# Kernel tuning notes

Measured on AMD Instinct MI355X. Metric: run time of the kernel, lower is better.

Reference implementation:

```python
import jax, jax.numpy as jnp
import numpy as np

B, M, D = 512, 100000, 256
EPS = 1e-8  # torch.cosine_similarity eps
TEMP = 10.0  # softmax temperature from source


def setup_inputs() -> dict:
    key = jax.random.key(0)
    kx, kk, kv = jax.random.split(key, 3)
    x = jax.random.normal(kx, (B, D), dtype=jnp.float32)
    memory_keys = jax.random.normal(kk, (M, D), dtype=jnp.float32) * 0.1
    memory_values = jax.random.normal(kv, (M, D), dtype=jnp.float32) * 0.1
    return {"x": x, "memory_keys": memory_keys, "memory_values": memory_values}


def reference(x, memory_keys, memory_values):
    # cosine similarity between x [B,D] and memory_keys [M,D] -> [B,M]
    dots = jnp.einsum("bd,md->bm", x, memory_keys)
    xn = jnp.linalg.norm(x, axis=-1)          # [B]
    kn = jnp.linalg.norm(memory_keys, axis=-1)  # [M]
    denom = jnp.maximum(xn[:, None] * kn[None, :], EPS)
    sims = dots / denom                         # [B,M]
    attn = jax.nn.softmax(sims * TEMP, axis=-1)  # [B,M]
    retrieved = jnp.einsum("bm,md->bd", attn, memory_values)  # [B,D]
    return retrieved, attn
```

## Files before the change

### kernel.cpp

```cpp
#include <hip/hip_runtime.h>
#include <hip/hip_bf16.h>


#define MCOLS 100000
#define MP    100032
#define DDIM  256
#define CHUNK 1792
#define NTFULL 28
#define NCHUNK 56
#define NST2  112
#define NSLOT 56
#define ATTN_OFF 131072
#define WS_RXN  0
#define WS_RKN  512
#define WS_RCPL 100512
#define WS_XB_BYTE   409600ull
#define WS_VT_BYTE   1048576ull
#define WS_PART_BYTE 52264960ull
#define WS_KB_BYTE   84246528ull
#define WS_KB_END    (WS_KB_BYTE + 2ull*(size_t)MCOLS*DDIM)

#define GLL(g, l) __builtin_amdgcn_global_load_lds( \
    (const __attribute__((address_space(1))) void*)(g), \
    (__attribute__((address_space(3))) void*)(l), 16, 0, 0)

typedef short short8 __attribute__((ext_vector_type(8)));
typedef float f32x4  __attribute__((ext_vector_type(4)));

static __device__ __forceinline__ unsigned short f2bfu(float f) {
  union { __hip_bfloat16 h; unsigned short u; } cv;
  cv.h = __float2bfloat16(f);
  return cv.u;
}
static __device__ __forceinline__ unsigned int pk2(float a, float b) {
  return (unsigned int)f2bfu(a) | ((unsigned int)f2bfu(b) << 16);
}
static __device__ __forceinline__ short8 pack8(float4 a, float4 b) {
  short8 r;
  r[0] = (short)f2bfu(a.x); r[1] = (short)f2bfu(a.y);
  r[2] = (short)f2bfu(a.z); r[3] = (short)f2bfu(a.w);
  r[4] = (short)f2bfu(b.x); r[5] = (short)f2bfu(b.y);
  r[6] = (short)f2bfu(b.z); r[7] = (short)f2bfu(b.w);
  return r;
}

__global__ void k0_xn(const float* __restrict__ x, float* __restrict__ ws) {
  const int b = blockIdx.x, t = threadIdx.x;
  const float v = x[b*DDIM + t];
  float s = v*v;
  #pragma unroll
  for (int mk = 1; mk <= 32; mk <<= 1) s += __shfl_xor(s, mk);
  __shared__ float ps[4];
  if ((t & 63) == 0) ps[t >> 6] = s;
  __syncthreads();
  const float tot = ps[0] + ps[1] + ps[2] + ps[3];
  const float r10 = 10.0f / fmaxf(sqrtf(tot), 1e-12f);
  if (t == 0) ws[WS_RXN + b] = r10;
  unsigned short* xbp = (unsigned short*)((char*)ws + WS_XB_BYTE);
  xbp[b*DDIM + t] = f2bfu(v * r10);
}

template<bool WRITEKB>
__global__ __launch_bounds__(256) void k0c_kn(const float* __restrict__ K,
                                              float* __restrict__ ws) {
  const int t = threadIdx.x;
  const int mg = blockIdx.x*64 + (t >> 2);
  const int qq = t & 3;
  if (mg >= MCOLS) return;
  const float* kp = K + (size_t)mg*DDIM + 64*qq;
  float4 buf[16];
  float ss = 0.f;
  #pragma unroll
  for (int j = 0; j < 16; ++j) {
    buf[j] = *(const float4*)(kp + 4*j);
    ss += buf[j].x*buf[j].x + buf[j].y*buf[j].y + buf[j].z*buf[j].z + buf[j].w*buf[j].w;
  }
  ss += __shfl_xor(ss, 1); ss += __shfl_xor(ss, 2);
  const float rk = 1.0f / fmaxf(sqrtf(ss), 1e-12f);
  if (qq == 0) ws[WS_RKN + mg] = rk;
  if (WRITEKB) {
    unsigned int* kb = (unsigned int*)((char*)ws + WS_KB_BYTE);
    #pragma unroll
    for (int j = 0; j < 8; ++j) {
      const float4 a = buf[2*j], b2 = buf[2*j+1];
      uint4 u;
      u.x = pk2(a.x*rk, a.y*rk);  u.y = pk2(a.z*rk, a.w*rk);
      u.z = pk2(b2.x*rk, b2.y*rk); u.w = pk2(b2.z*rk, b2.w*rk);
      const int slot = (8*qq + j) ^ (mg & 7);
      *(uint4*)(kb + (size_t)mg*128 + slot*4) = u;
    }
  }
}

__global__ __launch_bounds__(256) void k0b_tr(const float* __restrict__ V,
                                              float* __restrict__ ws) {
  const int t = threadIdx.x;
  const int m0 = blockIdx.x * 64;
  __shared__ float vt_f[64][261];
  #pragma unroll
  for (int i = 0; i < 4; ++i) {
    const int ml = (t >> 4) + 16*i;
    const int mg = m0 + ml;
    #pragma unroll
    for (int j = 0; j < 4; ++j) {
      const int d = 4*(t & 15) + 64*j;
      float4 v = make_float4(0.f, 0.f, 0.f, 0.f);
      if (mg < MCOLS) v = *(const float4*)(V + (size_t)mg*DDIM + d);
      vt_f[ml][d] = v.x; vt_f[ml][d+1] = v.y; vt_f[ml][d+2] = v.z; vt_f[ml][d+3] = v.w;
    }
  }
  __syncthreads();
  unsigned short* vt = (unsigned short*)((char*)ws + WS_VT_BYTE);
  const int tl = t & 15;
  const int s = tl >> 1, hf = tl & 1;
  const int mq = 8*s + 4*hf;
  #pragma unroll
  for (int it = 0; it < 16; ++it) {
    const int d = (t >> 4) + 16*it;
    uint2 u;
    u.x = pk2(vt_f[mq+0][d], vt_f[mq+1][d]);
    u.y = pk2(vt_f[mq+2][d], vt_f[mq+3][d]);
    const int sp = s ^ (d & 7);
    *(uint2*)(vt + (size_t)d*MP + m0 + sp*8 + 4*hf) = u;
  }
}

static __device__ __forceinline__ void stage_k(const char* __restrict__ kb,
                                               int m0, int w, int l,
                                               unsigned short (*klds)[256]) {
  #pragma unroll
  for (int i = 0; i < 4; ++i) {
    int r = m0 + w*8 + i*2 + (l >> 5);
    r = min(r, MCOLS - 1);
    const char* g = kb + (size_t)r*512 + (l & 31)*16;
    char* dst = (char*)&klds[w*8 + i*2][0];
    GLL(g, dst);
  }
}
static __device__ __forceinline__ void stage_vt(const char* __restrict__ vtb,
                                                int m1, int w, int l,
                                                unsigned short (*vtl)[64]) {
  #pragma unroll
  for (int i = 0; i < 4; ++i) {
    const int d = w*32 + i*8 + (l >> 3);
    const int ms = min(m1 + (l & 7)*8, MP - 8);
    const char* g = vtb + ((size_t)d*MP + ms)*2;
    char* dst = (char*)&vtl[w*32 + i*8][0];
    GLL(g, dst);
  }
}

__global__ __launch_bounds__(512, 4) void k1b_sum(const float* __restrict__ ws,
                                                  float* __restrict__ out) {
  const int bid = blockIdx.x;
  const int xg = bid & 7, i = bid >> 3;
  const int c = xg + 8*(i % 7), rb = i / 7;
  const int t = threadIdx.x, w = t >> 6, l = t & 63, q = l >> 4, ln = l & 15;
  const int ar = w & 3, h = w >> 2, l7 = ln & 7;
  __shared__ __align__(16) unsigned short klds2[2][64][256];
  const char* kb = (const char*)ws + WS_KB_BYTE;
  const unsigned short* xb = (const unsigned short*)((const char*)ws + WS_XB_BYTE);
  const int R0 = rb*64;

  short8 xf[8];
  {
    const int row = R0 + 16*ar + ln;
    #pragma unroll
    for (int kk = 0; kk < 8; ++kk)
      xf[kk] = *(const short8*)(xb + row*DDIM + 32*kk + 8*q);
  }
  float lpr[4] = {0.f,0.f,0.f,0.f};
  const int mbase = c*CHUNK;
  const int nt = min(NTFULL, (MCOLS - mbase + 63) >> 6);

  stage_k(kb, mbase, w, l, klds2[0]);
  __syncthreads();
  for (int mt = 0; mt < nt; ++mt) {
    const int cur = mt & 1;
    const int m0 = mbase + mt*64;
    if (mt + 1 < nt) stage_k(kb, m0 + 64, w, l, klds2[cur ^ 1]);
    const char* kbase = (const char*)&klds2[cur][0][0];
    const int row0 = 32*h + ln;
    f32x4 acc[2];
    { f32x4 z = {0.f,0.f,0.f,0.f}; acc[0] = z; acc[1] = z; }
    #pragma unroll
    for (int kk = 0; kk < 8; ++kk) {
      const int sl = ((q + 4*kk) ^ l7) << 4;
      const short8 b0 = *(const short8*)(kbase + row0*512 + sl);
      const short8 b1 = *(const short8*)(kbase + (row0 + 16)*512 + sl);
      acc[0] = __builtin_amdgcn_mfma_f32_16x16x32_bf16(xf[kk], b0, acc[0], 0,0,0);
      acc[1] = __builtin_amdgcn_mfma_f32_16x16x32_bf16(xf[kk], b1, acc[1], 0,0,0);
    }
    const int mr0 = m0 + row0, mr1 = mr0 + 16;
    const bool ok0 = mr0 < MCOLS, ok1 = mr1 < MCOLS;
    #pragma unroll
    for (int r = 0; r < 4; ++r)
      lpr[r] += (ok0 ? __expf(acc[0][r]) : 0.f) + (ok1 ? __expf(acc[1][r]) : 0.f);
    __syncthreads();
  }
  #pragma unroll
  for (int r = 0; r < 4; ++r) {
    float s = lpr[r];
    s += __shfl_xor(s, 1); s += __shfl_xor(s, 2);
    s += __shfl_xor(s, 4); s += __shfl_xor(s, 8);
    if (ln == 0)
      out[(size_t)(c*2 + h)*512 + R0 + 16*ar + 4*q + r] = s;
  }
}

__global__ void k2_final(const float* __restrict__ out, float* __restrict__ ws) {
  const int b = blockIdx.x, t = threadIdx.x;
  float v = (t < NST2) ? out[(size_t)t*512 + b] : 0.f;
  #pragma unroll
  for (int mk = 1; mk <= 32; mk <<= 1) v += __shfl_xor(v, mk);
  __shared__ float s2[2];
  if ((t & 63) == 0) s2[t >> 6] = v;
  __syncthreads();
  if (t == 0) ws[WS_RCPL + b] = 1.0f / (s2[0] + s2[1]);
}

__global__ __launch_bounds__(512, 4) void k3a_main(float* __restrict__ ws,
                                                   float* __restrict__ out) {
  const int bid = blockIdx.x;
  const int xg = bid & 7, i = bid >> 3;
  const int c = xg + 8*(i % 7), rb = i / 7;
  const int t = threadIdx.x, w = t >> 6, l = t & 63, q = l >> 4, ln = l & 15;
  const int ar = w & 3, h = w >> 2, l7 = ln & 15 & 7;
  __shared__ __align__(16) unsigned short klds[64][256];
  __shared__ __align__(16) unsigned short vtl[256][64];
  __shared__ __align__(16) unsigned short plds[64][64];
  const char* kb  = (const char*)ws + WS_KB_BYTE;
  const char* vtb = (const char*)ws + WS_VT_BYTE;
  const unsigned short* xb = (const unsigned short*)((const char*)ws + WS_XB_BYTE);
  const int R0 = rb*64;

  short8 xf[8];
  {
    const int row = R0 + 16*ar + ln;
    #pragma unroll
    for (int kk = 0; kk < 8; ++kk)
      xf[kk] = *(const short8*)(xb + row*DDIM + 32*kk + 8*q);
  }
  float rlq[4];
  #pragma unroll
  for (int r = 0; r < 4; ++r)
    rlq[r] = ws[WS_RCPL + R0 + 16*ar + 4*q + r];
  f32x4 apv[8];
  #pragma unroll
  for (int dx = 0; dx < 8; ++dx) { f32x4 z = {0.f,0.f,0.f,0.f}; apv[dx] = z; }
  const int d2 = 128*h;
  float* attn = out + ATTN_OFF;
  const int mbase = c*CHUNK;
  const int nt = min(NTFULL, (MCOLS - mbase + 63) >> 6);
  unsigned short* pf = &plds[0][0];

  stage_k(kb, mbase, w, l, klds);
  __syncthreads();

  for (int mt = 0; mt < nt; ++mt) {
    const int m0 = mbase + mt*64;
    stage_vt(vtb, m0, w, l, vtl);
    const int row0 = 32*h + ln;
    f32x4 acc[2];
    { f32x4 z = {0.f,0.f,0.f,0.f}; acc[0] = z; acc[1] = z; }
    #pragma unroll
    for (int kk = 0; kk < 8; ++kk) {
      const int sl = ((q + 4*kk) ^ l7) << 4;
      const short8 b0 = *(const short8*)((const char*)&klds[0][0] + row0*512 + sl);
      const short8 b1 = *(const short8*)((const char*)&klds[0][0] + (row0 + 16)*512 + sl);
      acc[0] = __builtin_amdgcn_mfma_f32_16x16x32_bf16(xf[kk], b0, acc[0], 0,0,0);
      acc[1] = __builtin_amdgcn_mfma_f32_16x16x32_bf16(xf[kk], b1, acc[1], 0,0,0);
    }
    const int mr0 = m0 + row0, mr1 = mr0 + 16;
    const bool ok0 = mr0 < MCOLS, ok1 = mr1 < MCOLS;
    #pragma unroll
    for (int r = 0; r < 4; ++r) {
      const int rowl = 16*ar + 4*q + r;
      const float p0v = ok0 ? __expf(acc[0][r]) : 0.f;
      const float p1v = ok1 ? __expf(acc[1][r]) : 0.f;
      float* arow = attn + (size_t)(R0 + rowl)*MCOLS;
      if (ok0) arow[mr0] = p0v*rlq[r];
      if (ok1) arow[mr1] = p1v*rlq[r];
      const int r7 = rowl & 7;
      pf[rowl*64 + ((((ln>>3) + 4*h    ) ^ r7) << 3) + (ln & 7)] = f2bfu(p0v);
      pf[rowl*64 + ((((ln>>3) + 4*h + 2) ^ r7) << 3) + (ln & 7)] = f2bfu(p1v);
    }
    __syncthreads();
    if (mt + 1 < nt) stage_k(kb, m0 + 64, w, l, klds);
    const int prow = 16*ar + ln;
    const short8 af0 = *(const short8*)(pf + prow*64 + ((q       ^ l7) << 3));
    const short8 af1 = *(const short8*)(pf + prow*64 + (((4 + q) ^ l7) << 3));
    #pragma unroll
    for (int dx = 0; dx < 8; ++dx) {
      const int R = d2 + 16*dx + ln;
      const char* vr = (const char*)&vtl[0][0] + R*128;
      const short8 bv0 = *(const short8*)(vr + ((q       ^ l7) << 4));
      const short8 bv1 = *(const short8*)(vr + (((4 + q) ^ l7) << 4));
      apv[dx] = __builtin_amdgcn_mfma_f32_16x16x32_bf16(af0, bv0, apv[dx], 0,0,0);
      apv[dx] = __builtin_amdgcn_mfma_f32_16x16x32_bf16(af1, bv1, apv[dx], 0,0,0);
    }
    __syncthreads();
  }

  float* part = (float*)((char*)ws + WS_PART_BYTE);
  #pragma unroll
  for (int dx = 0; dx < 8; ++dx)
    #pragma unroll
    for (int r = 0; r < 4; ++r)
      part[((size_t)c*512 + R0 + 16*ar + 4*q + r)*256 + d2 + 16*dx + ln]
        = apv[dx][r]*rlq[r];
}

static __device__ __forceinline__ void load_xf(const float* __restrict__ x,
                                               int brow0, int q, int ln,
                                               short8 xf[2][8]) {
  #pragma unroll
  for (int as = 0; as < 2; ++as) {
    const int row = brow0 + 16*as + ln;
    #pragma unroll
    for (int kk = 0; kk < 8; ++kk) {
      const float* p = x + row*DDIM + 32*kk + 8*q;
      xf[as][kk] = pack8(*(const float4*)p, *(const float4*)(p + 4));
    }
  }
}

__global__ __launch_bounds__(512, 2) void k3b_main(const float* __restrict__ x,
                                                   const float* __restrict__ K,
                                                   float* __restrict__ ws,
                                                   float* __restrict__ out) {
  const int bid = blockIdx.x;
  const int c = bid >> 2, rb = bid & 3;
  const int t = threadIdx.x, w = t >> 6, l = t & 63, q = l >> 4, ln = l & 15;
  const int h = w & 1, rg = w >> 1;
  __shared__ __align__(16) unsigned short plds[2][128][72];
  const int R0 = rb*128;
  short8 xf[2][8];
  const int brow0 = R0 + 32*rg;
  load_xf(x, brow0, q, ln, xf);
  float rxn[2][4];
  #pragma unroll
  for (int as = 0; as < 2; ++as)
    #pragma unroll
    for (int r = 0; r < 4; ++r)
      rxn[as][r] = ws[WS_RXN + brow0 + 16*as + 4*q + r];
  float lpr[2][4] = {{0.f,0.f,0.f,0.f},{0.f,0.f,0.f,0.f}};
  f32x4 apv[2][8];
  #pragma unroll
  for (int bs = 0; bs < 2; ++bs)
    #pragma unroll
    for (int dx = 0; dx < 8; ++dx) { f32x4 z = {0.f,0.f,0.f,0.f}; apv[bs][dx] = z; }
  const int b2 = 32*(w & 3), d2 = 128*(w >> 2);
  const unsigned short* vt = (const unsigned short*)((const char*)ws + WS_VT_BYTE);
  const float* rknw = ws + WS_RKN;
  float* attn = out + ATTN_OFF;
  const int mbase = c*CHUNK;
  const int nt = min(NTFULL, (MCOLS - mbase + 63) >> 6);
  const int l7 = ln & 7;

  for (int mt = 0; mt < nt; ++mt) {
    const int m0 = mbase + mt*64;
    const int mr0 = m0 + 32*h + ln, mr1 = mr0 + 16;
    const int kr0 = min(mr0, MCOLS-1), kr1 = min(mr1, MCOLS-1);
    f32x4 acc[2][2];
    #pragma unroll
    for (int as = 0; as < 2; ++as)
      #pragma unroll
      for (int mm = 0; mm < 2; ++mm) { f32x4 z = {0.f,0.f,0.f,0.f}; acc[as][mm] = z; }
    const float* p0 = K + (size_t)kr0*DDIM + 8*q;
    const float* p1 = K + (size_t)kr1*DDIM + 8*q;
    #pragma unroll
    for (int kk = 0; kk < 8; ++kk) {
      const short8 b0 = pack8(*(const float4*)(p0 + 32*kk), *(const float4*)(p0 + 32*kk + 4));
      const short8 b1 = pack8(*(const float4*)(p1 + 32*kk), *(const float4*)(p1 + 32*kk + 4));
      acc[0][0] = __builtin_amdgcn_mfma_f32_16x16x32_bf16(xf[0][kk], b0, acc[0][0], 0,0,0);
      acc[0][1] = __builtin_amdgcn_mfma_f32_16x16x32_bf16(xf[0][kk], b1, acc[0][1], 0,0,0);
      acc[1][0] = __builtin_amdgcn_mfma_f32_16x16x32_bf16(xf[1][kk], b0, acc[1][0], 0,0,0);
      acc[1][1] = __builtin_amdgcn_mfma_f32_16x16x32_bf16(xf[1][kk], b1, acc[1][1], 0,0,0);
    }
    const float rk0 = rknw[kr0], rk1 = rknw[kr1];
    const bool ok0 = mr0 < MCOLS, ok1 = mr1 < MCOLS;
    #pragma unroll
    for (int as = 0; as < 2; ++as)
      #pragma unroll
      for (int r = 0; r < 4; ++r) {
        const int rowl = 32*rg + 16*as + 4*q + r;
        const float p0v = ok0 ? __expf(acc[as][0][r]*rxn[as][r]*rk0) : 0.f;
        const float p1v = ok1 ? __expf(acc[as][1][r]*rxn[as][r]*rk1) : 0.f;
        float* arow = attn + (size_t)(R0 + rowl)*MCOLS;
        if (ok0) arow[mr0] = p0v;
        if (ok1) arow[mr1] = p1v;
        lpr[as][r] += p0v + p1v;
        plds[mt & 1][rowl][32*h + ln]      = f2bfu(p0v);
        plds[mt & 1][rowl][32*h + 16 + ln] = f2bfu(p1v);
      }
    __syncthreads();
    const unsigned short (*pb)[72] = plds[mt & 1];
    const short8 af00 = *(const short8*)&pb[b2 + ln][8*q];
    const short8 af01 = *(const short8*)&pb[b2 + ln][32 + 8*q];
    const short8 af10 = *(const short8*)&pb[b2 + 16 + ln][8*q];
    const short8 af11 = *(const short8*)&pb[b2 + 16 + ln][32 + 8*q];
    #pragma unroll
    for (int dx = 0; dx < 8; ++dx) {
      const int R = d2 + 16*dx + ln;
      const size_t rbase = (size_t)R*MP + m0;
      const short8 bv0 = *(const short8*)(vt + rbase + ((q     ^ (R & 7)) << 3));
      const short8 bv1 = *(const short8*)(vt + rbase + (((4+q) ^ (R & 7)) << 3));
      apv[0][dx] = __builtin_amdgcn_mfma_f32_16x16x32_bf16(af00, bv0, apv[0][dx], 0,0,0);
      apv[0][dx] = __builtin_amdgcn_mfma_f32_16x16x32_bf16(af01, bv1, apv[0][dx], 0,0,0);
      apv[1][dx] = __builtin_amdgcn_mfma_f32_16x16x32_bf16(af10, bv0, apv[1][dx], 0,0,0);
      apv[1][dx] = __builtin_amdgcn_mfma_f32_16x16x32_bf16(af11, bv1, apv[1][dx], 0,0,0);
    }
  }

  #pragma unroll
  for (int as = 0; as < 2; ++as)
    #pragma unroll
    for (int r = 0; r < 4; ++r) {
      float s = lpr[as][r];
      s += __shfl_xor(s, 1); s += __shfl_xor(s, 2);
      s += __shfl_xor(s, 4); s += __shfl_xor(s, 8);
      if (ln == 0)
        out[(size_t)(c*2 + h)*512 + brow0 + 16*as + 4*q + r] = s;
    }
  float* part = (float*)((char*)ws + WS_PART_BYTE);
  #pragma unroll
  for (int bs = 0; bs < 2; ++bs)
    #pragma unroll
    for (int dx = 0; dx < 8; ++dx)
      #pragma unroll
      for (int r = 0; r < 4; ++r)
        part[((size_t)c*512 + R0 + b2 + 16*bs + 4*q + r)*256 + d2 + 16*dx + ln]
          = apv[bs][dx][r];
}

template<bool NORM>
__global__ void k4_red(const float* __restrict__ ws, float* __restrict__ out) {
  const int b = blockIdx.x, t = threadIdx.x;
  const float* part = (const float*)((const char*)ws + WS_PART_BYTE);
  float acc = 0.f;
  for (int cc = 0; cc < NSLOT; ++cc)
    acc += part[((size_t)cc*512 + b)*256 + t];
  if (!NORM) acc *= ws[WS_RCPL + b];
  out[b*DDIM + t] = acc;
}

__global__ void k5_scale(const float* __restrict__ ws, float* __restrict__ out) {
  const int row = blockIdx.y;
  const int i4 = blockIdx.x*256 + threadIdx.x;
  if (i4 >= MCOLS/4) return;
  const float s = ws[WS_RCPL + row];
  float4* p = (float4*)(out + ATTN_OFF + (size_t)row*MCOLS) + i4;
  float4 v = *p;
  v.x *= s; v.y *= s; v.z *= s; v.w *= s;
  *p = v;
}

extern "C" void kernel_launch(void* const* d_in, const int* in_sizes, int n_in,
                              void* d_out, int out_size, void* d_ws, size_t ws_size,
                              hipStream_t stream) {
  const float* x = (const float*)d_in[0];
  const float* K = (const float*)d_in[1];
  const float* V = (const float*)d_in[2];
  float* out = (float*)d_out;
  float* ws  = (float*)d_ws;
  const bool useKB = ws_size >= WS_KB_END;

  k0_xn<<<512, 256, 0, stream>>>(x, ws);
  if (useKB) k0c_kn<true ><<<1563, 256, 0, stream>>>(K, ws);
  else       k0c_kn<false><<<1563, 256, 0, stream>>>(K, ws);
  k0b_tr<<<MP/64, 256, 0, stream>>>(V, ws);
  if (useKB) {
    k1b_sum<<<448, 512, 0, stream>>>(ws, out);
    k2_final<<<512, 128, 0, stream>>>(out, ws);
    k3a_main<<<448, 512, 0, stream>>>(ws, out);
    k4_red<true><<<512, 256, 0, stream>>>(ws, out);
  } else {
    k3b_main<<<224, 512, 0, stream>>>(x, K, ws, out);
    k2_final<<<512, 128, 0, stream>>>(out, ws);
    k5_scale<<<dim3((MCOLS/4 + 255)/256, 512), 256, 0, stream>>>(ws, out);
    k4_red<false><<<512, 256, 0, stream>>>(ws, out);
  }
}
```

Baseline: 250.2 us.

## Fuse softmax denominator pass into main kernel and normalize attention afterwards

Drops the separate exp-sum pass (k1b_sum) that recomputed x·K and exp before the main pass. The main kernel now accumulates the row sums itself and writes unnormalized exp values to attn and to the partial P·V buffers. k5_scale then rescales the full attention matrix, and k4_red applies the reciprocal to the retrieved output. The attn global stores are also moved after the barrier so they overlap with staging the next K tile. The trade-off is that one recompute of the similarity GEMM is exchanged for an extra read and write of the 512×100000 fp32 attention matrix.

```diff
diff --git a/kernel.cpp b/kernel.cpp
--- a/kernel.cpp
+++ b/kernel.cpp
@@ -150,82 +150,24 @@
   }
 }
 
-__global__ __launch_bounds__(512, 4) void k1b_sum(const float* __restrict__ ws,
-                                                  float* __restrict__ out) {
+__global__ void k2_final(const float* __restrict__ out, float* __restrict__ ws) {
+  const int b = blockIdx.x, t = threadIdx.x;
+  float v = (t < NST2) ? out[(size_t)t*512 + b] : 0.f;
+  #pragma unroll
+  for (int mk = 1; mk <= 32; mk <<= 1) v += __shfl_xor(v, mk);
+  __shared__ float s2[2];
+  if ((t & 63) == 0) s2[t >> 6] = v;
+  __syncthreads();
+  if (t == 0) ws[WS_RCPL + b] = 1.0f / (s2[0] + s2[1]);
+}
+
+__global__ __launch_bounds__(512, 4) void k3s_main(float* __restrict__ ws,
+                                                   float* __restrict__ out) {
   const int bid = blockIdx.x;
   const int xg = bid & 7, i = bid >> 3;
   const int c = xg + 8*(i % 7), rb = i / 7;
   const int t = threadIdx.x, w = t >> 6, l = t & 63, q = l >> 4, ln = l & 15;
   const int ar = w & 3, h = w >> 2, l7 = ln & 7;
-  __shared__ __align__(16) unsigned short klds2[2][64][256];
-  const char* kb = (const char*)ws + WS_KB_BYTE;
-  const unsigned short* xb = (const unsigned short*)((const char*)ws + WS_XB_BYTE);
-  const int R0 = rb*64;
-
-  short8 xf[8];
-  {
-    const int row = R0 + 16*ar + ln;
-    #pragma unroll
-    for (int kk = 0; kk < 8; ++kk)
-      xf[kk] = *(const short8*)(xb + row*DDIM + 32*kk + 8*q);
-  }
-  float lpr[4] = {0.f,0.f,0.f,0.f};
-  const int mbase = c*CHUNK;
-  const int nt = min(NTFULL, (MCOLS - mbase + 63) >> 6);
-
-  stage_k(kb, mbase, w, l, klds2[0]);
-  __syncthreads();
-  for (int mt = 0; mt < nt; ++mt) {
-    const int cur = mt & 1;
-    const int m0 = mbase + mt*64;
-    if (mt + 1 < nt) stage_k(kb, m0 + 64, w, l, klds2[cur ^ 1]);
-    const char* kbase = (const char*)&klds2[cur][0][0];
-    const int row0 = 32*h + ln;
-    f32x4 acc[2];
-    { f32x4 z = {0.f,0.f,0.f,0.f}; acc[0] = z; acc[1] = z; }
-    #pragma unroll
-    for (int kk = 0; kk < 8; ++kk) {
-      const int sl = ((q + 4*kk) ^ l7) << 4;
-      const short8 b0 = *(const short8*)(kbase + row0*512 + sl);
-      const short8 b1 = *(const short8*)(kbase + (row0 + 16)*512 + sl);
-      acc[0] = __builtin_amdgcn_mfma_f32_16x16x32_bf16(xf[kk], b0, acc[0], 0,0,0);
-      acc[1] = __builtin_amdgcn_mfma_f32_16x16x32_bf16(xf[kk], b1, acc[1], 0,0,0);
-    }
-    const int mr0 = m0 + row0, mr1 = mr0 + 16;
-    const bool ok0 = mr0 < MCOLS, ok1 = mr1 < MCOLS;
-    #pragma unroll
-    for (int r = 0; r < 4; ++r)
-      lpr[r] += (ok0 ? __expf(acc[0][r]) : 0.f) + (ok1 ? __expf(acc[1][r]) : 0.f);
-    __syncthreads();
-  }
-  #pragma unroll
-  for (int r = 0; r < 4; ++r) {
-    float s = lpr[r];
-    s += __shfl_xor(s, 1); s += __shfl_xor(s, 2);
-    s += __shfl_xor(s, 4); s += __shfl_xor(s, 8);
-    if (ln == 0)
-      out[(size_t)(c*2 + h)*512 + R0 + 16*ar + 4*q + r] = s;
-  }
-}
-
-__global__ void k2_final(const float* __restrict__ out, float* __restrict__ ws) {
-  const int b = blockIdx.x, t = threadIdx.x;
-  float v = (t < NST2) ? out[(size_t)t*512 + b] : 0.f;
-  #pragma unroll
-  for (int mk = 1; mk <= 32; mk <<= 1) v += __shfl_xor(v, mk);
-  __shared__ float s2[2];
-  if ((t & 63) == 0) s2[t >> 6] = v;
-  __syncthreads();
-  if (t == 0) ws[WS_RCPL + b] = 1.0f / (s2[0] + s2[1]);
-}
-
-__global__ __launch_bounds__(512, 4) void k3a_main(float* __restrict__ ws,
-                                                   float* __restrict__ out) {
-  const int bid = blockIdx.x;
-  const int xg = bid & 7, i = bid >> 3;
-  const int c = xg + 8*(i % 7), rb = i / 7;
-  const int t = threadIdx.x, w = t >> 6, l = t & 63, q = l >> 4, ln = l & 15;
-  const int ar = w & 3, h = w >> 2, l7 = ln & 15 & 7;
   __shared__ __align__(16) unsigned short klds[64][256];
   __shared__ __align__(16) unsigned short vtl[256][64];
   __shared__ __align__(16) unsigned short plds[64][64];
@@ -241,10 +183,7 @@
     for (int kk = 0; kk < 8; ++kk)
       xf[kk] = *(const short8*)(xb + row*DDIM + 32*kk + 8*q);
   }
-  float rlq[4];
-  #pragma unroll
-  for (int r = 0; r < 4; ++r)
-    rlq[r] = ws[WS_RCPL + R0 + 16*ar + 4*q + r];
+  float lpr[4] = {0.f,0.f,0.f,0.f};
   f32x4 apv[8];
   #pragma unroll
   for (int dx = 0; dx < 8; ++dx) { f32x4 z = {0.f,0.f,0.f,0.f}; apv[dx] = z; }
@@ -273,20 +212,27 @@
     }
     const int mr0 = m0 + row0, mr1 = mr0 + 16;
     const bool ok0 = mr0 < MCOLS, ok1 = mr1 < MCOLS;
+    float pv0[4], pv1[4];
     #pragma unroll
     for (int r = 0; r < 4; ++r) {
       const int rowl = 16*ar + 4*q + r;
       const float p0v = ok0 ? __expf(acc[0][r]) : 0.f;
       const float p1v = ok1 ? __expf(acc[1][r]) : 0.f;
-      float* arow = attn + (size_t)(R0 + rowl)*MCOLS;
-      if (ok0) arow[mr0] = p0v*rlq[r];
-      if (ok1) arow[mr1] = p1v*rlq[r];
+      pv0[r] = p0v; pv1[r] = p1v;
+      lpr[r] += p0v + p1v;
       const int r7 = rowl & 7;
       pf[rowl*64 + ((((ln>>3) + 4*h    ) ^ r7) << 3) + (ln & 7)] = f2bfu(p0v);
       pf[rowl*64 + ((((ln>>3) + 4*h + 2) ^ r7) << 3) + (ln & 7)] = f2bfu(p1v);
     }
     __syncthreads();
     if (mt + 1 < nt) stage_k(kb, m0 + 64, w, l, klds);
+    #pragma unroll
+    for (int r = 0; r < 4; ++r) {
+      const int rowl = 16*ar + 4*q + r;
+      float* arow = attn + (size_t)(R0 + rowl)*MCOLS;
+      if (ok0) arow[mr0] = pv0[r];
+      if (ok1) arow[mr1] = pv1[r];
+    }
     const int prow = 16*ar + ln;
     const short8 af0 = *(const short8*)(pf + prow*64 + ((q       ^ l7) << 3));
     const short8 af1 = *(const short8*)(pf + prow*64 + (((4 + q) ^ l7) << 3));
@@ -302,13 +248,21 @@
     __syncthreads();
   }
 
+  #pragma unroll
+  for (int r = 0; r < 4; ++r) {
+    float s = lpr[r];
+    s += __shfl_xor(s, 1); s += __shfl_xor(s, 2);
+    s += __shfl_xor(s, 4); s += __shfl_xor(s, 8);
+    if (ln == 0)
+      out[(size_t)(c*2 + h)*512 + R0 + 16*ar + 4*q + r] = s;
+  }
   float* part = (float*)((char*)ws + WS_PART_BYTE);
   #pragma unroll
   for (int dx = 0; dx < 8; ++dx)
     #pragma unroll
     for (int r = 0; r < 4; ++r)
       part[((size_t)c*512 + R0 + 16*ar + 4*q + r)*256 + d2 + 16*dx + ln]
-        = apv[dx][r]*rlq[r];
+        = apv[dx][r];
 }
 
 static __device__ __forceinline__ void load_xf(const float* __restrict__ x,
@@ -434,15 +388,13 @@
           = apv[bs][dx][r];
 }
 
-template<bool NORM>
 __global__ void k4_red(const float* __restrict__ ws, float* __restrict__ out) {
   const int b = blockIdx.x, t = threadIdx.x;
   const float* part = (const float*)((const char*)ws + WS_PART_BYTE);
   float acc = 0.f;
   for (int cc = 0; cc < NSLOT; ++cc)
     acc += part[((size_t)cc*512 + b)*256 + t];
-  if (!NORM) acc *= ws[WS_RCPL + b];
-  out[b*DDIM + t] = acc;
+  out[b*DDIM + t] = acc * ws[WS_RCPL + b];
 }
 
 __global__ void k5_scale(const float* __restrict__ ws, float* __restrict__ out) {
@@ -470,15 +422,9 @@
   if (useKB) k0c_kn<true ><<<1563, 256, 0, stream>>>(K, ws);
   else       k0c_kn<false><<<1563, 256, 0, stream>>>(K, ws);
   k0b_tr<<<MP/64, 256, 0, stream>>>(V, ws);
-  if (useKB) {
-    k1b_sum<<<448, 512, 0, stream>>>(ws, out);
-    k2_final<<<512, 128, 0, stream>>>(out, ws);
-    k3a_main<<<448, 512, 0, stream>>>(ws, out);
-    k4_red<true><<<512, 256, 0, stream>>>(ws, out);
-  } else {
-    k3b_main<<<224, 512, 0, stream>>>(x, K, ws, out);
-    k2_final<<<512, 128, 0, stream>>>(out, ws);
-    k5_scale<<<dim3((MCOLS/4 + 255)/256, 512), 256, 0, stream>>>(ws, out);
-    k4_red<false><<<512, 256, 0, stream>>>(ws, out);
-  }
-}
+  if (useKB) k3s_main<<<448, 512, 0, stream>>>(ws, out);
+  else       k3b_main<<<224, 512, 0, stream>>>(x, K, ws, out);
+  k2_final<<<512, 128, 0, stream>>>(out, ws);
+  k5_scale<<<dim3((MCOLS/4 + 255)/256, 512), 256, 0, stream>>>(ws, out);
+  k4_red<<<512, 256, 0, stream>>>(ws, out);
+}
```

After: 337.0 us. 34.7% more time.

## Split row-sum kernel into smaller 32-row tiles across more blocks

Applied to the files above, without the earlier changes.

The exp-sum pass now uses 128 chunks of 832 key rows processed in 32-row tiles, launched as 1024 blocks instead of 448 blocks with 64-row tiles. The LDS staging buffer is halved and launch bounds are raised to allow 8 waves per SIMD, aiming at better occupancy and GPU fill. The final reduction kernel is templated on the number of partial sums and widened to 256 threads. In exchange, each block does less work per synchronisation and repeats the per-block load of the x fragments, and there are more partial sums to reduce.

```diff
diff --git a/kernel.cpp b/kernel.cpp
--- a/kernel.cpp
+++ b/kernel.cpp
@@ -8,8 +8,10 @@
 #define CHUNK 1792
 #define NTFULL 28
 #define NCHUNK 56
-#define NST2  112
 #define NSLOT 56
+#define CHUNK1 832
+#define NT1   26
+#define NCH1  128
 #define ATTN_OFF 131072
 #define WS_RXN  0
 #define WS_RKN  512
@@ -137,6 +139,18 @@
     GLL(g, dst);
   }
 }
+static __device__ __forceinline__ void stage_k32(const char* __restrict__ kb,
+                                                 int m0, int w, int l,
+                                                 unsigned short (*klds)[256]) {
+  #pragma unroll
+  for (int i = 0; i < 2; ++i) {
+    int r = m0 + w*4 + i*2 + (l >> 5);
+    r = min(r, MCOLS - 1);
+    const char* g = kb + (size_t)r*512 + (l & 31)*16;
+    char* dst = (char*)&klds[w*4 + i*2][0];
+    GLL(g, dst);
+  }
+}
 static __device__ __forceinline__ void stage_vt(const char* __restrict__ vtb,
                                                 int m1, int w, int l,
                                                 unsigned short (*vtl)[64]) {
@@ -150,14 +164,14 @@
   }
 }
 
-__global__ __launch_bounds__(512, 4) void k1b_sum(const float* __restrict__ ws,
+__global__ __launch_bounds__(512, 8) void k1b_sum(const float* __restrict__ ws,
                                                   float* __restrict__ out) {
   const int bid = blockIdx.x;
   const int xg = bid & 7, i = bid >> 3;
-  const int c = xg + 8*(i % 7), rb = i / 7;
+  const int c = xg + 8*(i & 15), rb = i >> 4;
   const int t = threadIdx.x, w = t >> 6, l = t & 63, q = l >> 4, ln = l & 15;
   const int ar = w & 3, h = w >> 2, l7 = ln & 7;
-  __shared__ __align__(16) unsigned short klds2[2][64][256];
+  __shared__ __align__(16) unsigned short klds2[2][32][256];
   const char* kb = (const char*)ws + WS_KB_BYTE;
   const unsigned short* xb = (const unsigned short*)((const char*)ws + WS_XB_BYTE);
   const int R0 = rb*64;
@@ -170,33 +184,33 @@
       xf[kk] = *(const short8*)(xb + row*DDIM + 32*kk + 8*q);
   }
   float lpr[4] = {0.f,0.f,0.f,0.f};
-  const int mbase = c*CHUNK;
-  const int nt = min(NTFULL, (MCOLS - mbase + 63) >> 6);
-
-  stage_k(kb, mbase, w, l, klds2[0]);
-  __syncthreads();
-  for (int mt = 0; mt < nt; ++mt) {
-    const int cur = mt & 1;
-    const int m0 = mbase + mt*64;
-    if (mt + 1 < nt) stage_k(kb, m0 + 64, w, l, klds2[cur ^ 1]);
-    const char* kbase = (const char*)&klds2[cur][0][0];
-    const int row0 = 32*h + ln;
-    f32x4 acc[2];
-    { f32x4 z = {0.f,0.f,0.f,0.f}; acc[0] = z; acc[1] = z; }
-    #pragma unroll
-    for (int kk = 0; kk < 8; ++kk) {
-      const int sl = ((q + 4*kk) ^ l7) << 4;
-      const short8 b0 = *(const short8*)(kbase + row0*512 + sl);
-      const short8 b1 = *(const short8*)(kbase + (row0 + 16)*512 + sl);
-      acc[0] = __builtin_amdgcn_mfma_f32_16x16x32_bf16(xf[kk], b0, acc[0], 0,0,0);
-      acc[1] = __builtin_amdgcn_mfma_f32_16x16x32_bf16(xf[kk], b1, acc[1], 0,0,0);
-    }
-    const int mr0 = m0 + row0, mr1 = mr0 + 16;
-    const bool ok0 = mr0 < MCOLS, ok1 = mr1 < MCOLS;
-    #pragma unroll
-    for (int r = 0; r < 4; ++r)
-      lpr[r] += (ok0 ? __expf(acc[0][r]) : 0.f) + (ok1 ? __expf(acc[1][r]) : 0.f);
+  const int mbase = c*CHUNK1;
+  const int rem = MCOLS - mbase;
+  const int nt = rem <= 0 ? 0 : min(NT1, (rem + 31) >> 5);
+
+  if (nt > 0) {
+    stage_k32(kb, mbase, w, l, klds2[0]);
     __syncthreads();
+    for (int mt = 0; mt < nt; ++mt) {
+      const int cur = mt & 1;
+      const int m0 = mbase + mt*32;
+      if (mt + 1 < nt) stage_k32(kb, m0 + 32, w, l, klds2[cur ^ 1]);
+      const char* kbase = (const char*)&klds2[cur][0][0];
+      const int row0 = 16*h + ln;
+      f32x4 acc = {0.f,0.f,0.f,0.f};
+      #pragma unroll
+      for (int kk = 0; kk < 8; ++kk) {
+        const int sl = ((q + 4*kk) ^ l7) << 4;
+        const short8 b0 = *(const short8*)(kbase + row0*512 + sl);
+        acc = __builtin_amdgcn_mfma_f32_16x16x32_bf16(xf[kk], b0, acc, 0,0,0);
+      }
+      const int mr = m0 + row0;
+      const bool ok = mr < MCOLS;
+      #pragma unroll
+      for (int r = 0; r < 4; ++r)
+        lpr[r] += ok ? __expf(acc[r]) : 0.f;
+      __syncthreads();
+    }
   }
   #pragma unroll
   for (int r = 0; r < 4; ++r) {
@@ -208,15 +222,16 @@
   }
 }
 
+template<int NSUM>
 __global__ void k2_final(const float* __restrict__ out, float* __restrict__ ws) {
   const int b = blockIdx.x, t = threadIdx.x;
-  float v = (t < NST2) ? out[(size_t)t*512 + b] : 0.f;
+  float v = (t < NSUM) ? out[(size_t)t*512 + b] : 0.f;
   #pragma unroll
   for (int mk = 1; mk <= 32; mk <<= 1) v += __shfl_xor(v, mk);
-  __shared__ float s2[2];
+  __shared__ float s2[4];
   if ((t & 63) == 0) s2[t >> 6] = v;
   __syncthreads();
-  if (t == 0) ws[WS_RCPL + b] = 1.0f / (s2[0] + s2[1]);
+  if (t == 0) ws[WS_RCPL + b] = 1.0f / (s2[0] + s2[1] + s2[2] + s2[3]);
 }
 
 __global__ __launch_bounds__(512, 4) void k3a_main(float* __restrict__ ws,
@@ -225,7 +240,7 @@
   const int xg = bid & 7, i = bid >> 3;
   const int c = xg + 8*(i % 7), rb = i / 7;
   const int t = threadIdx.x, w = t >> 6, l = t & 63, q = l >> 4, ln = l & 15;
-  const int ar = w & 3, h = w >> 2, l7 = ln & 15 & 7;
+  const int ar = w & 3, h = w >> 2, l7 = ln & 7;
   __shared__ __align__(16) unsigned short klds[64][256];
   __shared__ __align__(16) unsigned short vtl[256][64];
   __shared__ __align__(16) unsigned short plds[64][64];
@@ -471,13 +486,13 @@
   else       k0c_kn<false><<<1563, 256, 0, stream>>>(K, ws);
   k0b_tr<<<MP/64, 256, 0, stream>>>(V, ws);
   if (useKB) {
-    k1b_sum<<<448, 512, 0, stream>>>(ws, out);
-    k2_final<<<512, 128, 0, stream>>>(out, ws);
+    k1b_sum<<<1024, 512, 0, stream>>>(ws, out);
+    k2_final<256><<<512, 256, 0, stream>>>(out, ws);
     k3a_main<<<448, 512, 0, stream>>>(ws, out);
     k4_red<true><<<512, 256, 0, stream>>>(ws, out);
   } else {
     k3b_main<<<224, 512, 0, stream>>>(x, K, ws, out);
-    k2_final<<<512, 128, 0, stream>>>(out, ws);
+    k2_final<112><<<512, 256, 0, stream>>>(out, ws);
     k5_scale<<<dim3((MCOLS/4 + 255)/256, 512), 256, 0, stream>>>(ws, out);
     k4_red<false><<<512, 256, 0, stream>>>(ws, out);
   }
```

New measurement: 253.1 us. About the same (+1.1%).
